# Performance work log

Measured on AMD Instinct MI355X. Metric: run time of the kernel, lower is better.

The kernel has to match this reference:

```python
import jax, jax.numpy as jnp
import numpy as np

B, N, FIN, H, F = 8, 1024, 256, 8, 64
NEG_SLOPE = 0.2


def setup_inputs() -> dict:
    key = jax.random.key(0)
    k = jax.random.split(key, 6)
    x = jax.random.normal(k[0], (B, N, FIN), dtype=jnp.float32)
    adj_mask = jax.random.randint(k[1], (B, N, N), 0, 2, dtype=jnp.int32)
    edge_prior = jax.random.normal(k[2], (B, N, N), dtype=jnp.float32)
    # params (xavier-style scales)
    W = jax.random.normal(k[3], (FIN, H * F), dtype=jnp.float32) * np.sqrt(2.0 / (FIN + H * F))
    a_left = jax.random.normal(k[4], (H, F), dtype=jnp.float32) * np.sqrt(2.0 / (1 + F))
    a_right = jax.random.normal(k[5], (H, F), dtype=jnp.float32) * np.sqrt(2.0 / (1 + F))
    edge_scale = jnp.float32(0.05)
    return {"x": x, "adj_mask": adj_mask, "edge_prior": edge_prior,
            "W": W, "a_left": a_left, "a_right": a_right, "edge_scale": edge_scale}


def reference(x, adj_mask, edge_prior, W, a_left, a_right, edge_scale):
    b, n, _ = x.shape
    h = (x @ W).reshape(b, n, H, F)                      # [B,N,H,F]
    e_left = jnp.einsum('bnhf,hf->bnh', h, a_left)       # [B,N,H]
    e_right = jnp.einsum('bnhf,hf->bnh', h, a_right)     # [B,N,H]
    e = jax.nn.leaky_relu(e_left[:, :, None, :] + e_right[:, None, :, :],
                          negative_slope=NEG_SLOPE)      # [B,N,N,H]
    e = e + edge_scale * edge_prior[..., None]
    e = jnp.where((adj_mask == 0)[..., None], -jnp.inf, e)
    alpha = jax.nn.softmax(e, axis=2)                    # softmax over neighbors j
    h_new = jnp.einsum('bijh,bjhf->bihf', alpha, h)      # [B,N,H,F]
    return h_new.reshape(b, n, H * F)                    # concat=True
```

## Files before the change

### kernel.cpp

```cpp
#include <hip/hip_runtime.h>
#include <hip/hip_bf16.h>

#define B_ 8
#define N_ 1024
#define FIN_ 256
#define H_ 8
#define F_ 64
#define HF_ 512
#define BN_ 8192
#define LOG2E 1.4426950408889634f

using bf16x8 = __attribute__((ext_vector_type(8))) short;
using f32x4  = __attribute__((ext_vector_type(4))) float;
using i32x4  = __attribute__((ext_vector_type(4))) int;

__device__ __forceinline__ short f2bf(float x) {
  __hip_bfloat16 b = __float2bfloat16(x);
  return *reinterpret_cast<short*>(&b);
}
__device__ __forceinline__ float bf2f(short s) {
  union { unsigned u; float f; } v;
  v.u = ((unsigned)(unsigned short)s) << 16;
  return v.f;
}
__device__ __forceinline__ bf16x8 cvtCE(f32x4 pa, f32x4 pb, i32x4 ma, i32x4 mb, float es) {
  bf16x8 o;
#pragma unroll
  for (int e = 0; e < 4; e++) {
    o[e]     = f2bf(ma[e] != 0 ? es * pa[e] : -1e30f);
    o[e + 4] = f2bf(mb[e] != 0 ? es * pb[e] : -1e30f);
  }
  return o;
}

__global__ __launch_bounds__(256) void k_cvt(
    const float* __restrict__ x, const float* __restrict__ W,
    short* __restrict__ xb, short* __restrict__ Wt) {
  const int bid = blockIdx.x;
  if (bid < 1024) {
    const int idx = (bid * 256 + threadIdx.x) * 8;
    f32x4 a = *(const f32x4*)(x + idx);
    f32x4 b = *(const f32x4*)(x + idx + 4);
    bf16x8 o;
    o[0]=f2bf(a[0]); o[1]=f2bf(a[1]); o[2]=f2bf(a[2]); o[3]=f2bf(a[3]);
    o[4]=f2bf(b[0]); o[5]=f2bf(b[1]); o[6]=f2bf(b[2]); o[7]=f2bf(b[3]);
    *(bf16x8*)(xb + idx) = o;
  } else {
    const int idx = (bid - 1024) * 256 + threadIdx.x;
    const int f = idx >> 8, c = idx & 255;
    Wt[f * FIN_ + c] = f2bf(W[c * HF_ + f]);
  }
}

__global__ __launch_bounds__(256) void k_h(
    const short* __restrict__ Wt, const short* __restrict__ xb,
    const float* __restrict__ aL, const float* __restrict__ aR,
    short* __restrict__ hAg, float* __restrict__ el_t, float* __restrict__ er_t) {
  const int nt = blockIdx.x;
  const int h  = blockIdx.y;
  const int w  = threadIdx.x >> 6;
  const int l  = threadIdx.x & 63;
  const int lr = l & 15, lk = l >> 4;
  const int n0 = nt * 64;
  const int fbase = h * 64 + w * 16;

  f32x4 acc[4] = {};
  const short* arow = Wt + (fbase + lr) * FIN_ + lk * 8;

#pragma unroll
  for (int k0 = 0; k0 < FIN_; k0 += 32) {
    bf16x8 a = *(const bf16x8*)(arow + k0);
#pragma unroll
    for (int nf = 0; nf < 4; nf++) {
      bf16x8 bb = *(const bf16x8*)(xb + (size_t)(n0 + nf * 16 + lr) * FIN_ + k0 + lk * 8);
      acc[nf] = __builtin_amdgcn_mfma_f32_16x16x32_bf16(a, bb, acc[nf], 0, 0, 0);
    }
  }

  __shared__ short sT[64][72];
  __shared__ float sEl[4][64], sEr[4][64];
  float al[4], ar[4];
#pragma unroll
  for (int r = 0; r < 4; r++) {
    const int fl = w * 16 + lk * 4 + r;
    al[r] = aL[h * F_ + fl];
    ar[r] = aR[h * F_ + fl];
  }
#pragma unroll
  for (int nf = 0; nf < 4; nf++) {
    const int nl = nf * 16 + lr;
#pragma unroll
    for (int r = 0; r < 4; r++)
      sT[w * 16 + lk * 4 + r][nl] = f2bf(acc[nf][r]);
    float pl = acc[nf][0]*al[0] + acc[nf][1]*al[1] + acc[nf][2]*al[2] + acc[nf][3]*al[3];
    float pr = acc[nf][0]*ar[0] + acc[nf][1]*ar[1] + acc[nf][2]*ar[2] + acc[nf][3]*ar[3];
    pl += __shfl_xor(pl, 16); pl += __shfl_xor(pl, 32);
    pr += __shfl_xor(pr, 16); pr += __shfl_xor(pr, 32);
    if (lk == 0) { sEl[w][nl] = pl; sEr[w][nl] = pr; }
  }
  __syncthreads();
  if (threadIdx.x < 64) {
    const int n = threadIdx.x;
    el_t[h * BN_ + n0 + n] = (sEl[0][n] + sEl[1][n] + sEl[2][n] + sEl[3][n]) * LOG2E;
    er_t[h * BN_ + n0 + n] = (sEr[0][n] + sEr[1][n] + sEr[2][n] + sEr[3][n]) * LOG2E;
  }
  const int b8h = (nt >> 4) * 8 + h;
  const int jb  = (nt & 15) * 2;
#pragma unroll
  for (int gi = 0; gi < 2; gi++) {
    const int g   = threadIdx.x * 2 + gi;
    const int jsl = g >> 8, ff = (g >> 6) & 3, gl = g & 63;
    const int glr = gl & 15, glk = gl >> 4;
    bf16x8 v = *(const bf16x8*)(&sT[ff * 16 + glr][jsl * 32 + glk * 8]);
    *(bf16x8*)(hAg + (((size_t)b8h * 32 + jb + jsl) * 4 + ff) * 512 + gl * 8) = v;
  }
}

#define PREF_G(sn, Hd, E0d, E1d)                                      \
  {                                                                   \
    const short* hs_ = hW + (size_t)(sn) * 2048;                      \
    Hd[0] = *(const bf16x8*)(hs_);                                    \
    Hd[1] = *(const bf16x8*)(hs_ + 512);                              \
    Hd[2] = *(const bf16x8*)(hs_ + 1024);                             \
    Hd[3] = *(const bf16x8*)(hs_ + 1536);                             \
    E0d   = *(const f32x4*)(erp + (sn) * 32);                         \
    E1d   = *(const f32x4*)(erp + (sn) * 32 + 4);                     \
  }

#define PREF_C(sn, C0d, C1d)                                          \
  {                                                                   \
    const int gi_ = (((sn) * 4 + lk) ^ xsw) * 8;                      \
    C0d = *(const bf16x8*)(cbl0 + gi_);                               \
    C1d = *(const bf16x8*)(cbl1 + gi_);                               \
  }

#define COMP2(Hu, C0u, C1u, E0u, E1u)                                          \
  {                                                                            \
    bf16x8 pfA, pfB;                                                           \
    _Pragma("unroll")                                                          \
    for (int q = 0; q < 4; q++) {                                              \
      const float e0 = E0u[q], e1 = E1u[q];                                    \
      float sA  = el0 + e0, sA2 = el0 + e1;                                    \
      float sB  = el1 + e0, sB2 = el1 + e1;                                    \
      float vA  = fmaf(0.6f, sA,  bf2f(C0u[q]));                               \
      vA  = fmaf(0.4f, fabsf(sA),  vA);                                        \
      float vA2 = fmaf(0.6f, sA2, bf2f(C0u[q + 4]));                           \
      vA2 = fmaf(0.4f, fabsf(sA2), vA2);                                       \
      float vB  = fmaf(0.6f, sB,  bf2f(C1u[q]));                               \
      vB  = fmaf(0.4f, fabsf(sB),  vB);                                        \
      float vB2 = fmaf(0.6f, sB2, bf2f(C1u[q + 4]));                           \
      vB2 = fmaf(0.4f, fabsf(sB2), vB2);                                       \
      float x1_, x2_, x3_, x4_;                                                \
      asm("v_exp_f32 %0, %1" : "=v"(x1_) : "v"(vA));                           \
      asm("v_exp_f32 %0, %1" : "=v"(x2_) : "v"(vA2));                          \
      asm("v_exp_f32 %0, %1" : "=v"(x3_) : "v"(vB));                           \
      asm("v_exp_f32 %0, %1" : "=v"(x4_) : "v"(vB2));                          \
      pfA[q] = f2bf(x1_); pfA[q + 4] = f2bf(x2_);                              \
      pfB[q] = f2bf(x3_); pfB[q + 4] = f2bf(x4_);                              \
    }                                                                          \
    accSA   = __builtin_amdgcn_mfma_f32_16x16x32_bf16(ones, pfA, accSA, 0,0,0);\
    accSB   = __builtin_amdgcn_mfma_f32_16x16x32_bf16(ones, pfB, accSB, 0,0,0);\
    accA[0] = __builtin_amdgcn_mfma_f32_16x16x32_bf16(Hu[0], pfA, accA[0],0,0,0);\
    accB[0] = __builtin_amdgcn_mfma_f32_16x16x32_bf16(Hu[0], pfB, accB[0],0,0,0);\
    accA[1] = __builtin_amdgcn_mfma_f32_16x16x32_bf16(Hu[1], pfA, accA[1],0,0,0);\
    accB[1] = __builtin_amdgcn_mfma_f32_16x16x32_bf16(Hu[1], pfB, accB[1],0,0,0);\
    accA[2] = __builtin_amdgcn_mfma_f32_16x16x32_bf16(Hu[2], pfA, accA[2],0,0,0);\
    accB[2] = __builtin_amdgcn_mfma_f32_16x16x32_bf16(Hu[2], pfB, accB[2],0,0,0);\
    accA[3] = __builtin_amdgcn_mfma_f32_16x16x32_bf16(Hu[3], pfA, accA[3],0,0,0);\
    accB[3] = __builtin_amdgcn_mfma_f32_16x16x32_bf16(Hu[3], pfB, accB[3],0,0,0);\
  }

__global__ __launch_bounds__(256, 2) void k_attn(
    const short* __restrict__ hAg, const float* __restrict__ el_t,
    const float* __restrict__ er_t, const float* __restrict__ prior,
    const int* __restrict__ mask, const float* __restrict__ esp,
    float* __restrict__ out) {
  const int bid = blockIdx.x;
  const int b  = bid & 7;
  const int hp = (bid >> 3) & 1;
  const int it = bid >> 4;
  const int t  = threadIdx.x;
  const int h  = hp * 4 + (t >> 6);
  const int l  = t & 63;
  const int lr = l & 15, lk = l >> 4;
  const int i0 = it * 32;
  const size_t bn = (size_t)b * N_;
  const float es = esp[0] * LOG2E;

  __shared__ short cbuf[33 * 1024];

  {
    const int srow = t >> 3;
    const int g0   = t & 7;
    const int sw   = srow & 7;
    const size_t grow = (bn + i0 + srow) * (size_t)N_;
    const float* pg = prior + grow;
    const int*   mg = mask  + grow;
#pragma unroll
    for (int k = 0; k < 16; k++) {
      const int g = g0 + 8 * k;
      f32x4 p0 = *(const f32x4*)(pg + g * 8), p1 = *(const f32x4*)(pg + g * 8 + 4);
      i32x4 m0 = *(const i32x4*)(mg + g * 8), m1 = *(const i32x4*)(mg + g * 8 + 4);
      *(bf16x8*)(&cbuf[srow * 1024 + (g ^ sw) * 8]) = cvtCE(p0, p1, m0, m1, es);
    }
  }

  const float el0 = el_t[h * BN_ + bn + i0 + lr];
  const float el1 = el_t[h * BN_ + bn + i0 + 16 + lr];
  const float* erp = er_t + h * BN_ + bn + lk * 8;
  const short* hW  = hAg + (size_t)(b * 8 + h) * 65536 + l * 8;
  const short* cbl0 = cbuf + lr * 1024;
  const short* cbl1 = cbuf + (16 + lr) * 1024;
  const int xsw = lr & 7;

  bf16x8 HA[4], HB[4], cA0, cA1, cB0, cB1;
  f32x4 eA0, eA1, eB0, eB1;

  PREF_G(0, HA, eA0, eA1);
  PREF_G(1, HB, eB0, eB1);

  f32x4 accA[4] = {}, accB[4] = {};
  f32x4 accSA = {}, accSB = {};
  bf16x8 ones;
#pragma unroll
  for (int e = 0; e < 8; e++) ones[e] = (short)0x3F80;

  __syncthreads();
  PREF_C(0, cA0, cA1);
  PREF_C(1, cB0, cB1);

  for (int s = 0; s < 32; s += 2) {
    COMP2(HA, cA0, cA1, eA0, eA1);
    PREF_G(s + 2, HA, eA0, eA1);
    PREF_C(s + 2, cA0, cA1);
    COMP2(HB, cB0, cB1, eB0, eB1);
    PREF_G(s + 3, HB, eB0, eB1);
    PREF_C(s + 3, cB0, cB1);
  }

  const float invA = 1.0f / accSA[0];
  const float invB = 1.0f / accSB[0];
  const size_t rowA = bn + i0 + lr;
  const size_t rowB = rowA + 16;
#pragma unroll
  for (int ff = 0; ff < 4; ff++) {
    f32x4 va = accA[ff], vb = accB[ff];
    va[0]*=invA; va[1]*=invA; va[2]*=invA; va[3]*=invA;
    vb[0]*=invB; vb[1]*=invB; vb[2]*=invB; vb[3]*=invB;
    *(f32x4*)(out + rowA * HF_ + h * 64 + ff * 16 + lk * 4) = va;
    *(f32x4*)(out + rowB * HF_ + h * 64 + ff * 16 + lk * 4) = vb;
  }
}

extern "C" void kernel_launch(void* const* d_in, const int* in_sizes, int n_in,
                              void* d_out, int out_size, void* d_ws, size_t ws_size,
                              hipStream_t stream) {
  const float* x     = (const float*)d_in[0];
  const int*   adj   = (const int*)  d_in[1];
  const float* prior = (const float*)d_in[2];
  const float* W     = (const float*)d_in[3];
  const float* aL    = (const float*)d_in[4];
  const float* aR    = (const float*)d_in[5];
  const float* es    = (const float*)d_in[6];
  float* out = (float*)d_out;

  char* ws = (char*)d_ws;
  short* hAg  = (short*)ws;
  short* xb   = (short*)(ws + 8u  * 1024 * 1024);
  short* Wt   = (short*)(ws + 12u * 1024 * 1024);
  float* el_t = (float*)(ws + 12u * 1024 * 1024 + 262144);
  float* er_t = (float*)(ws + 12u * 1024 * 1024 + 524288);

  hipLaunchKernelGGL(k_cvt, dim3(1536), dim3(256), 0, stream, x, W, xb, Wt);
  hipLaunchKernelGGL(k_h,   dim3(128, 8), dim3(256), 0, stream,
                     Wt, xb, aL, aR, hAg, el_t, er_t);
  hipLaunchKernelGGL(k_attn, dim3(512), dim3(256), 0, stream,
                     hAg, el_t, er_t, prior, adj, es, out);
}
```

Measured before the change: 65.82 us.

## Double-buffer prior/mask staging in 256-column chunks with 64-row tiles

The attention kernel now handles 64 query rows per block instead of 32, which halves the grid and doubles the reuse of each loaded H tile across four MFMA row groups. The prior/mask tile is staged in four 256-column chunks into two shared buffers, so the global loads for the next chunk are interleaved with compute on the current one. This replaces the old single up-front load of the full 32x1024 tile. MFMA blocks are wrapped in s_setprio. The risks are higher register pressure from 16 accumulators, 256 blocks possibly underfilling the CUs, and extra barriers.

New measurement: 69.87 us. 1.06x slower.

```diff
diff --git a/kernel.cpp b/kernel.cpp
--- a/kernel.cpp
+++ b/kernel.cpp
@@ -127,47 +127,71 @@
     E1d   = *(const f32x4*)(erp + (sn) * 32 + 4);                     \
   }
 
-#define PREF_C(sn, C0d, C1d)                                          \
-  {                                                                   \
-    const int gi_ = (((sn) * 4 + lk) ^ xsw) * 8;                      \
-    C0d = *(const bf16x8*)(cbl0 + gi_);                               \
-    C1d = *(const bf16x8*)(cbl1 + gi_);                               \
-  }
-
-#define COMP2(Hu, C0u, C1u, E0u, E1u)                                          \
-  {                                                                            \
-    bf16x8 pfA, pfB;                                                           \
-    _Pragma("unroll")                                                          \
-    for (int q = 0; q < 4; q++) {                                              \
-      const float e0 = E0u[q], e1 = E1u[q];                                    \
-      float sA  = el0 + e0, sA2 = el0 + e1;                                    \
-      float sB  = el1 + e0, sB2 = el1 + e1;                                    \
-      float vA  = fmaf(0.6f, sA,  bf2f(C0u[q]));                               \
-      vA  = fmaf(0.4f, fabsf(sA),  vA);                                        \
-      float vA2 = fmaf(0.6f, sA2, bf2f(C0u[q + 4]));                           \
-      vA2 = fmaf(0.4f, fabsf(sA2), vA2);                                       \
-      float vB  = fmaf(0.6f, sB,  bf2f(C1u[q]));                               \
-      vB  = fmaf(0.4f, fabsf(sB),  vB);                                        \
-      float vB2 = fmaf(0.6f, sB2, bf2f(C1u[q + 4]));                           \
-      vB2 = fmaf(0.4f, fabsf(sB2), vB2);                                       \
-      float x1_, x2_, x3_, x4_;                                                \
-      asm("v_exp_f32 %0, %1" : "=v"(x1_) : "v"(vA));                           \
-      asm("v_exp_f32 %0, %1" : "=v"(x2_) : "v"(vA2));                          \
-      asm("v_exp_f32 %0, %1" : "=v"(x3_) : "v"(vB));                           \
-      asm("v_exp_f32 %0, %1" : "=v"(x4_) : "v"(vB2));                          \
-      pfA[q] = f2bf(x1_); pfA[q + 4] = f2bf(x2_);                              \
-      pfB[q] = f2bf(x3_); pfB[q + 4] = f2bf(x4_);                              \
-    }                                                                          \
-    accSA   = __builtin_amdgcn_mfma_f32_16x16x32_bf16(ones, pfA, accSA, 0,0,0);\
-    accSB   = __builtin_amdgcn_mfma_f32_16x16x32_bf16(ones, pfB, accSB, 0,0,0);\
-    accA[0] = __builtin_amdgcn_mfma_f32_16x16x32_bf16(Hu[0], pfA, accA[0],0,0,0);\
-    accB[0] = __builtin_amdgcn_mfma_f32_16x16x32_bf16(Hu[0], pfB, accB[0],0,0,0);\
-    accA[1] = __builtin_amdgcn_mfma_f32_16x16x32_bf16(Hu[1], pfA, accA[1],0,0,0);\
-    accB[1] = __builtin_amdgcn_mfma_f32_16x16x32_bf16(Hu[1], pfB, accB[1],0,0,0);\
-    accA[2] = __builtin_amdgcn_mfma_f32_16x16x32_bf16(Hu[2], pfA, accA[2],0,0,0);\
-    accB[2] = __builtin_amdgcn_mfma_f32_16x16x32_bf16(Hu[2], pfB, accB[2],0,0,0);\
-    accA[3] = __builtin_amdgcn_mfma_f32_16x16x32_bf16(Hu[3], pfA, accA[3],0,0,0);\
-    accB[3] = __builtin_amdgcn_mfma_f32_16x16x32_bf16(Hu[3], pfB, accB[3],0,0,0);\
+#define PREF_C4(cbp, js, Cd)                                          \
+  {                                                                   \
+    const int gi_ = (((js) * 4 + lk) ^ xsw) * 8;                      \
+    Cd[0] = *(const bf16x8*)((cbp) + lr * 256 + gi_);                 \
+    Cd[1] = *(const bf16x8*)((cbp) + (16 + lr) * 256 + gi_);          \
+    Cd[2] = *(const bf16x8*)((cbp) + (32 + lr) * 256 + gi_);          \
+    Cd[3] = *(const bf16x8*)((cbp) + (48 + lr) * 256 + gi_);          \
+  }
+
+#define SLOAD(ch1, js)                                                \
+  {                                                                   \
+    const float* pp_ = rowp + (ch1) * 256 + (js) * 8;                 \
+    const int*   mm_ = rowm + (ch1) * 256 + (js) * 8;                 \
+    sp0 = *(const f32x4*)(pp_); sp1 = *(const f32x4*)(pp_ + 4);       \
+    sm0 = *(const i32x4*)(mm_); sm1 = *(const i32x4*)(mm_ + 4);       \
+  }
+
+#define SWRITE(bufp, js)                                              \
+  {                                                                   \
+    *(bf16x8*)((bufp) + rbase + (((sgrp + (js)) ^ rsw) * 8)) =        \
+        cvtCE(sp0, sp1, sm0, sm1, es);                                \
+  }
+
+#define LGT(elv, ee, cc, dst)                                         \
+  {                                                                   \
+    float t_ = (elv) + (ee);                                          \
+    float v_ = fmaf(0.4f, fabsf(t_), fmaf(0.6f, t_, bf2f(cc)));       \
+    float x_;                                                         \
+    asm("v_exp_f32 %0, %1" : "=v"(x_) : "v"(v_));                     \
+    dst = f2bf(x_);                                                   \
+  }
+
+#define COMP4(Hu, Cu, E0u, E1u)                                                 \
+  {                                                                             \
+    bf16x8 pf0, pf1, pf2, pf3;                                                  \
+    _Pragma("unroll")                                                           \
+    for (int q = 0; q < 4; q++) {                                               \
+      const float e0 = E0u[q], e1 = E1u[q];                                     \
+      LGT(el0, e0, Cu[0][q], pf0[q]); LGT(el0, e1, Cu[0][q + 4], pf0[q + 4]);   \
+      LGT(el1, e0, Cu[1][q], pf1[q]); LGT(el1, e1, Cu[1][q + 4], pf1[q + 4]);   \
+      LGT(el2, e0, Cu[2][q], pf2[q]); LGT(el2, e1, Cu[2][q + 4], pf2[q + 4]);   \
+      LGT(el3, e0, Cu[3][q], pf3[q]); LGT(el3, e1, Cu[3][q + 4], pf3[q + 4]);   \
+    }                                                                           \
+    __builtin_amdgcn_s_setprio(1);                                              \
+    accS[0] = __builtin_amdgcn_mfma_f32_16x16x32_bf16(ones, pf0, accS[0],0,0,0);\
+    accS[1] = __builtin_amdgcn_mfma_f32_16x16x32_bf16(ones, pf1, accS[1],0,0,0);\
+    accS[2] = __builtin_amdgcn_mfma_f32_16x16x32_bf16(ones, pf2, accS[2],0,0,0);\
+    accS[3] = __builtin_amdgcn_mfma_f32_16x16x32_bf16(ones, pf3, accS[3],0,0,0);\
+    acc[0][0] = __builtin_amdgcn_mfma_f32_16x16x32_bf16(Hu[0], pf0, acc[0][0],0,0,0);\
+    acc[0][1] = __builtin_amdgcn_mfma_f32_16x16x32_bf16(Hu[0], pf1, acc[0][1],0,0,0);\
+    acc[0][2] = __builtin_amdgcn_mfma_f32_16x16x32_bf16(Hu[0], pf2, acc[0][2],0,0,0);\
+    acc[0][3] = __builtin_amdgcn_mfma_f32_16x16x32_bf16(Hu[0], pf3, acc[0][3],0,0,0);\
+    acc[1][0] = __builtin_amdgcn_mfma_f32_16x16x32_bf16(Hu[1], pf0, acc[1][0],0,0,0);\
+    acc[1][1] = __builtin_amdgcn_mfma_f32_16x16x32_bf16(Hu[1], pf1, acc[1][1],0,0,0);\
+    acc[1][2] = __builtin_amdgcn_mfma_f32_16x16x32_bf16(Hu[1], pf2, acc[1][2],0,0,0);\
+    acc[1][3] = __builtin_amdgcn_mfma_f32_16x16x32_bf16(Hu[1], pf3, acc[1][3],0,0,0);\
+    acc[2][0] = __builtin_amdgcn_mfma_f32_16x16x32_bf16(Hu[2], pf0, acc[2][0],0,0,0);\
+    acc[2][1] = __builtin_amdgcn_mfma_f32_16x16x32_bf16(Hu[2], pf1, acc[2][1],0,0,0);\
+    acc[2][2] = __builtin_amdgcn_mfma_f32_16x16x32_bf16(Hu[2], pf2, acc[2][2],0,0,0);\
+    acc[2][3] = __builtin_amdgcn_mfma_f32_16x16x32_bf16(Hu[2], pf3, acc[2][3],0,0,0);\
+    acc[3][0] = __builtin_amdgcn_mfma_f32_16x16x32_bf16(Hu[3], pf0, acc[3][0],0,0,0);\
+    acc[3][1] = __builtin_amdgcn_mfma_f32_16x16x32_bf16(Hu[3], pf1, acc[3][1],0,0,0);\
+    acc[3][2] = __builtin_amdgcn_mfma_f32_16x16x32_bf16(Hu[3], pf2, acc[3][2],0,0,0);\
+    acc[3][3] = __builtin_amdgcn_mfma_f32_16x16x32_bf16(Hu[3], pf3, acc[3][3],0,0,0);\
+    __builtin_amdgcn_s_setprio(0);                                              \
   }
 
 __global__ __launch_bounds__(256, 2) void k_attn(
@@ -183,72 +207,93 @@
   const int h  = hp * 4 + (t >> 6);
   const int l  = t & 63;
   const int lr = l & 15, lk = l >> 4;
-  const int i0 = it * 32;
+  const int i0 = it * 64;
   const size_t bn = (size_t)b * N_;
   const float es = esp[0] * LOG2E;
 
-  __shared__ short cbuf[33 * 1024];
-
-  {
-    const int srow = t >> 3;
-    const int g0   = t & 7;
-    const int sw   = srow & 7;
-    const size_t grow = (bn + i0 + srow) * (size_t)N_;
-    const float* pg = prior + grow;
-    const int*   mg = mask  + grow;
-#pragma unroll
-    for (int k = 0; k < 16; k++) {
-      const int g = g0 + 8 * k;
-      f32x4 p0 = *(const f32x4*)(pg + g * 8), p1 = *(const f32x4*)(pg + g * 8 + 4);
-      i32x4 m0 = *(const i32x4*)(mg + g * 8), m1 = *(const i32x4*)(mg + g * 8 + 4);
-      *(bf16x8*)(&cbuf[srow * 1024 + (g ^ sw) * 8]) = cvtCE(p0, p1, m0, m1, es);
-    }
-  }
-
-  const float el0 = el_t[h * BN_ + bn + i0 + lr];
-  const float el1 = el_t[h * BN_ + bn + i0 + 16 + lr];
+  __shared__ short cbuf[2][16384];
+
+  const int r    = t >> 2;
+  const int sub  = t & 3;
+  const int rbase = r * 256;
+  const int rsw  = r & 7;
+  const int sgrp = sub * 8;
+  const float* rowp = prior + (bn + i0 + r) * (size_t)N_ + sub * 64;
+  const int*   rowm = mask  + (bn + i0 + r) * (size_t)N_ + sub * 64;
+  f32x4 sp0, sp1; i32x4 sm0, sm1;
+
+  const float* elh = el_t + h * BN_ + bn + i0;
+  const float el0 = elh[lr], el1 = elh[16 + lr], el2 = elh[32 + lr], el3 = elh[48 + lr];
   const float* erp = er_t + h * BN_ + bn + lk * 8;
   const short* hW  = hAg + (size_t)(b * 8 + h) * 65536 + l * 8;
-  const short* cbl0 = cbuf + lr * 1024;
-  const short* cbl1 = cbuf + (16 + lr) * 1024;
   const int xsw = lr & 7;
 
-  bf16x8 HA[4], HB[4], cA0, cA1, cB0, cB1;
+  bf16x8 HA[4], HB[4], cA[4], cB[4];
   f32x4 eA0, eA1, eB0, eB1;
-
+  f32x4 acc[4][4] = {};
+  f32x4 accS[4] = {};
+  bf16x8 ones;
+#pragma unroll
+  for (int e = 0; e < 8; e++) ones[e] = (short)0x3F80;
+
+#pragma unroll
+  for (int g = 0; g < 8; g++) {
+    SLOAD(0, g);
+    SWRITE(&cbuf[0][0], g);
+  }
   PREF_G(0, HA, eA0, eA1);
   PREF_G(1, HB, eB0, eB1);
-
-  f32x4 accA[4] = {}, accB[4] = {};
-  f32x4 accSA = {}, accSB = {};
-  bf16x8 ones;
-#pragma unroll
-  for (int e = 0; e < 8; e++) ones[e] = (short)0x3F80;
-
   __syncthreads();
-  PREF_C(0, cA0, cA1);
-  PREF_C(1, cB0, cB1);
-
-  for (int s = 0; s < 32; s += 2) {
-    COMP2(HA, cA0, cA1, eA0, eA1);
-    PREF_G(s + 2, HA, eA0, eA1);
-    PREF_C(s + 2, cA0, cA1);
-    COMP2(HB, cB0, cB1, eB0, eB1);
-    PREF_G(s + 3, HB, eB0, eB1);
-    PREF_C(s + 3, cB0, cB1);
-  }
-
-  const float invA = 1.0f / accSA[0];
-  const float invB = 1.0f / accSB[0];
-  const size_t rowA = bn + i0 + lr;
-  const size_t rowB = rowA + 16;
-#pragma unroll
-  for (int ff = 0; ff < 4; ff++) {
-    f32x4 va = accA[ff], vb = accB[ff];
-    va[0]*=invA; va[1]*=invA; va[2]*=invA; va[3]*=invA;
-    vb[0]*=invB; vb[1]*=invB; vb[2]*=invB; vb[3]*=invB;
-    *(f32x4*)(out + rowA * HF_ + h * 64 + ff * 16 + lk * 4) = va;
-    *(f32x4*)(out + rowB * HF_ + h * 64 + ff * 16 + lk * 4) = vb;
+  PREF_C4(&cbuf[0][0], 0, cA);
+  PREF_C4(&cbuf[0][0], 1, cB);
+
+  for (int ch = 0; ch < 4; ++ch) {
+    const int s0 = ch * 8;
+    const short* cbc = &cbuf[ch & 1][0];
+    short*       cbn = &cbuf[(ch + 1) & 1][0];
+    const bool stg = (ch < 3);
+    if (stg) { SLOAD(ch + 1, 0); }
+    COMP4(HA, cA, eA0, eA1);
+    PREF_G(s0 + 2, HA, eA0, eA1);  PREF_C4(cbc, 2, cA);
+    if (stg) { SWRITE(cbn, 0); SLOAD(ch + 1, 1); }
+    COMP4(HB, cB, eB0, eB1);
+    PREF_G(s0 + 3, HB, eB0, eB1);  PREF_C4(cbc, 3, cB);
+    if (stg) { SWRITE(cbn, 1); SLOAD(ch + 1, 2); }
+    COMP4(HA, cA, eA0, eA1);
+    PREF_G(s0 + 4, HA, eA0, eA1);  PREF_C4(cbc, 4, cA);
+    if (stg) { SWRITE(cbn, 2); SLOAD(ch + 1, 3); }
+    COMP4(HB, cB, eB0, eB1);
+    PREF_G(s0 + 5, HB, eB0, eB1);  PREF_C4(cbc, 5, cB);
+    if (stg) { SWRITE(cbn, 3); SLOAD(ch + 1, 4); }
+    COMP4(HA, cA, eA0, eA1);
+    PREF_G(s0 + 6, HA, eA0, eA1);  PREF_C4(cbc, 6, cA);
+    if (stg) { SWRITE(cbn, 4); SLOAD(ch + 1, 5); }
+    COMP4(HB, cB, eB0, eB1);
+    PREF_G(s0 + 7, HB, eB0, eB1);  PREF_C4(cbc, 7, cB);
+    if (stg) { SWRITE(cbn, 5); SLOAD(ch + 1, 6); }
+    COMP4(HA, cA, eA0, eA1);
+    { const int sn_ = (s0 + 8 > 31) ? 31 : s0 + 8; PREF_G(sn_, HA, eA0, eA1); }
+    if (stg) { SWRITE(cbn, 6); SLOAD(ch + 1, 7); }
+    COMP4(HB, cB, eB0, eB1);
+    { const int sn_ = (s0 + 9 > 31) ? 31 : s0 + 9; PREF_G(sn_, HB, eB0, eB1); }
+    if (stg) {
+      SWRITE(cbn, 7);
+      __syncthreads();
+      PREF_C4(cbn, 0, cA);
+      PREF_C4(cbn, 1, cB);
+    }
+  }
+
+#pragma unroll
+  for (int fi = 0; fi < 4; fi++) {
+    const float inv = 1.0f / accS[fi][0];
+    const size_t row = bn + i0 + fi * 16 + lr;
+#pragma unroll
+    for (int ff = 0; ff < 4; ff++) {
+      f32x4 v = acc[ff][fi];
+      v[0] *= inv; v[1] *= inv; v[2] *= inv; v[3] *= inv;
+      *(f32x4*)(out + row * HF_ + h * 64 + ff * 16 + lk * 4) = v;
+    }
   }
 }
 
@@ -274,6 +319,6 @@
   hipLaunchKernelGGL(k_cvt, dim3(1536), dim3(256), 0, stream, x, W, xb, Wt);
   hipLaunchKernelGGL(k_h,   dim3(128, 8), dim3(256), 0, stream,
                      Wt, xb, aL, aR, hAg, el_t, er_t);
-  hipLaunchKernelGGL(k_attn, dim3(512), dim3(256), 0, stream,
+  hipLaunchKernelGGL(k_attn, dim3(256), dim3(256), 0, stream,
                      hAg, el_t, er_t, prior, adj, es, out);
 }
```

## Precompute prior/mask bias into MFMA-layout bf16 buffer via separate kernel

Applied to the files above, without the earlier changes.

Moves the fp32 prior plus int mask to bf16 bias conversion out of the attention kernel into a new k_pre kernel. k_pre writes the bias into a global buffer already laid out in MFMA fragment order. The attention kernel then streams these fragments straight from global memory alongside h and er, with no LDS staging or __syncthreads. Its software prefetch deepens from two stages to four, and the MFMA block is wrapped in s_setprio. The intent is to remove the LDS prologue and raise occupancy. The cost is an extra kernel launch and a 16 MB bf16 write-then-read round trip through memory.

New measurement: 67.29 us. +2.2%, slower.

```diff
diff --git a/kernel.cpp b/kernel.cpp
--- a/kernel.cpp
+++ b/kernel.cpp
@@ -52,6 +52,30 @@
   }
 }
 
+__global__ __launch_bounds__(256) void k_pre(
+    const float* __restrict__ prior, const int* __restrict__ mask,
+    const float* __restrict__ esp, short* __restrict__ cmat) {
+  const int b  = blockIdx.x & 7;
+  const int it = blockIdx.x >> 3;
+  const int t  = threadIdx.x;
+  const int i  = t >> 3;
+  const int jb = (t & 7) * 8;
+  const float es = esp[0] * LOG2E;
+  const size_t rowbase = ((size_t)b * N_ + it * 32 + i) * N_;
+  short* cmt = cmat + (size_t)(b * 32 + it) * 32768
+             + (i >> 4) * 512 + (i & 15) * 8;
+#pragma unroll
+  for (int jt = 0; jt < 16; jt++) {
+    const int j = jt * 64 + jb;
+    f32x4 p0 = *(const f32x4*)(prior + rowbase + j);
+    f32x4 p1 = *(const f32x4*)(prior + rowbase + j + 4);
+    i32x4 m0 = *(const i32x4*)(mask + rowbase + j);
+    i32x4 m1 = *(const i32x4*)(mask + rowbase + j + 4);
+    *(bf16x8*)(cmt + (j >> 5) * 1024 + ((j >> 3) & 3) * 128) =
+        cvtCE(p0, p1, m0, m1, es);
+  }
+}
+
 __global__ __launch_bounds__(256) void k_h(
     const short* __restrict__ Wt, const short* __restrict__ xb,
     const float* __restrict__ aL, const float* __restrict__ aR,
@@ -116,7 +140,7 @@
   }
 }
 
-#define PREF_G(sn, Hd, E0d, E1d)                                      \
+#define PREFX(sn, Hd, E0d, E1d, Cd)                                   \
   {                                                                   \
     const short* hs_ = hW + (size_t)(sn) * 2048;                      \
     Hd[0] = *(const bf16x8*)(hs_);                                    \
@@ -125,16 +149,11 @@
     Hd[3] = *(const bf16x8*)(hs_ + 1536);                             \
     E0d   = *(const f32x4*)(erp + (sn) * 32);                         \
     E1d   = *(const f32x4*)(erp + (sn) * 32 + 4);                     \
-  }
-
-#define PREF_C(sn, C0d, C1d)                                          \
-  {                                                                   \
-    const int gi_ = (((sn) * 4 + lk) ^ xsw) * 8;                      \
-    C0d = *(const bf16x8*)(cbl0 + gi_);                               \
-    C1d = *(const bf16x8*)(cbl1 + gi_);                               \
-  }
-
-#define COMP2(Hu, C0u, C1u, E0u, E1u)                                          \
+    Cd[0] = *(const bf16x8*)(cmW + (size_t)(sn) * 1024);              \
+    Cd[1] = *(const bf16x8*)(cmW + (size_t)(sn) * 1024 + 512);        \
+  }
+
+#define COMP2(Hu, Cu, E0u, E1u)                                                \
   {                                                                            \
     bf16x8 pfA, pfB;                                                           \
     _Pragma("unroll")                                                          \
@@ -142,13 +161,13 @@
       const float e0 = E0u[q], e1 = E1u[q];                                    \
       float sA  = el0 + e0, sA2 = el0 + e1;                                    \
       float sB  = el1 + e0, sB2 = el1 + e1;                                    \
-      float vA  = fmaf(0.6f, sA,  bf2f(C0u[q]));                               \
+      float vA  = fmaf(0.6f, sA,  bf2f(Cu[0][q]));                             \
       vA  = fmaf(0.4f, fabsf(sA),  vA);                                        \
-      float vA2 = fmaf(0.6f, sA2, bf2f(C0u[q + 4]));                           \
+      float vA2 = fmaf(0.6f, sA2, bf2f(Cu[0][q + 4]));                         \
       vA2 = fmaf(0.4f, fabsf(sA2), vA2);                                       \
-      float vB  = fmaf(0.6f, sB,  bf2f(C1u[q]));                               \
+      float vB  = fmaf(0.6f, sB,  bf2f(Cu[1][q]));                             \
       vB  = fmaf(0.4f, fabsf(sB),  vB);                                        \
-      float vB2 = fmaf(0.6f, sB2, bf2f(C1u[q + 4]));                           \
+      float vB2 = fmaf(0.6f, sB2, bf2f(Cu[1][q + 4]));                         \
       vB2 = fmaf(0.4f, fabsf(sB2), vB2);                                       \
       float x1_, x2_, x3_, x4_;                                                \
       asm("v_exp_f32 %0, %1" : "=v"(x1_) : "v"(vA));                           \
@@ -158,6 +177,7 @@
       pfA[q] = f2bf(x1_); pfA[q + 4] = f2bf(x2_);                              \
       pfB[q] = f2bf(x3_); pfB[q + 4] = f2bf(x4_);                              \
     }                                                                          \
+    __builtin_amdgcn_s_setprio(1);                                             \
     accSA   = __builtin_amdgcn_mfma_f32_16x16x32_bf16(ones, pfA, accSA, 0,0,0);\
     accSB   = __builtin_amdgcn_mfma_f32_16x16x32_bf16(ones, pfB, accSB, 0,0,0);\
     accA[0] = __builtin_amdgcn_mfma_f32_16x16x32_bf16(Hu[0], pfA, accA[0],0,0,0);\
@@ -168,12 +188,12 @@
     accB[2] = __builtin_amdgcn_mfma_f32_16x16x32_bf16(Hu[2], pfB, accB[2],0,0,0);\
     accA[3] = __builtin_amdgcn_mfma_f32_16x16x32_bf16(Hu[3], pfA, accA[3],0,0,0);\
     accB[3] = __builtin_amdgcn_mfma_f32_16x16x32_bf16(Hu[3], pfB, accB[3],0,0,0);\
+    __builtin_amdgcn_s_setprio(0);                                             \
   }
 
 __global__ __launch_bounds__(256, 2) void k_attn(
     const short* __restrict__ hAg, const float* __restrict__ el_t,
-    const float* __restrict__ er_t, const float* __restrict__ prior,
-    const int* __restrict__ mask, const float* __restrict__ esp,
+    const float* __restrict__ er_t, const short* __restrict__ cmat,
     float* __restrict__ out) {
   const int bid = blockIdx.x;
   const int b  = bid & 7;
@@ -185,57 +205,32 @@
   const int lr = l & 15, lk = l >> 4;
   const int i0 = it * 32;
   const size_t bn = (size_t)b * N_;
-  const float es = esp[0] * LOG2E;
-
-  __shared__ short cbuf[33 * 1024];
-
-  {
-    const int srow = t >> 3;
-    const int g0   = t & 7;
-    const int sw   = srow & 7;
-    const size_t grow = (bn + i0 + srow) * (size_t)N_;
-    const float* pg = prior + grow;
-    const int*   mg = mask  + grow;
-#pragma unroll
-    for (int k = 0; k < 16; k++) {
-      const int g = g0 + 8 * k;
-      f32x4 p0 = *(const f32x4*)(pg + g * 8), p1 = *(const f32x4*)(pg + g * 8 + 4);
-      i32x4 m0 = *(const i32x4*)(mg + g * 8), m1 = *(const i32x4*)(mg + g * 8 + 4);
-      *(bf16x8*)(&cbuf[srow * 1024 + (g ^ sw) * 8]) = cvtCE(p0, p1, m0, m1, es);
-    }
-  }
 
   const float el0 = el_t[h * BN_ + bn + i0 + lr];
   const float el1 = el_t[h * BN_ + bn + i0 + 16 + lr];
   const float* erp = er_t + h * BN_ + bn + lk * 8;
   const short* hW  = hAg + (size_t)(b * 8 + h) * 65536 + l * 8;
-  const short* cbl0 = cbuf + lr * 1024;
-  const short* cbl1 = cbuf + (16 + lr) * 1024;
-  const int xsw = lr & 7;
-
-  bf16x8 HA[4], HB[4], cA0, cA1, cB0, cB1;
-  f32x4 eA0, eA1, eB0, eB1;
-
-  PREF_G(0, HA, eA0, eA1);
-  PREF_G(1, HB, eB0, eB1);
-
+  const short* cmW = cmat + (size_t)(b * 32 + it) * 32768 + l * 8;
+
+  bf16x8 HA[4], HB[4], HC[4], HD[4];
+  bf16x8 cA[2], cB[2], cC[2], cD[2];
+  f32x4 eA0, eA1, eB0, eB1, eC0, eC1, eD0, eD1;
   f32x4 accA[4] = {}, accB[4] = {};
   f32x4 accSA = {}, accSB = {};
   bf16x8 ones;
 #pragma unroll
   for (int e = 0; e < 8; e++) ones[e] = (short)0x3F80;
 
-  __syncthreads();
-  PREF_C(0, cA0, cA1);
-  PREF_C(1, cB0, cB1);
-
-  for (int s = 0; s < 32; s += 2) {
-    COMP2(HA, cA0, cA1, eA0, eA1);
-    PREF_G(s + 2, HA, eA0, eA1);
-    PREF_C(s + 2, cA0, cA1);
-    COMP2(HB, cB0, cB1, eB0, eB1);
-    PREF_G(s + 3, HB, eB0, eB1);
-    PREF_C(s + 3, cB0, cB1);
+  PREFX(0, HA, eA0, eA1, cA);
+  PREFX(1, HB, eB0, eB1, cB);
+  PREFX(2, HC, eC0, eC1, cC);
+  PREFX(3, HD, eD0, eD1, cD);
+
+  for (int s = 0; s < 32; s += 4) {
+    COMP2(HA, cA, eA0, eA1);  PREFX(s + 4, HA, eA0, eA1, cA);
+    COMP2(HB, cB, eB0, eB1);  PREFX(s + 5, HB, eB0, eB1, cB);
+    COMP2(HC, cC, eC0, eC1);  PREFX(s + 6, HC, eC0, eC1, cC);
+    COMP2(HD, cD, eD0, eD1);  PREFX(s + 7, HD, eD0, eD1, cD);
   }
 
   const float invA = 1.0f / accSA[0];
@@ -270,10 +265,12 @@
   short* Wt   = (short*)(ws + 12u * 1024 * 1024);
   float* el_t = (float*)(ws + 12u * 1024 * 1024 + 262144);
   float* er_t = (float*)(ws + 12u * 1024 * 1024 + 524288);
+  short* cmat = (short*)(ws + 13u * 1024 * 1024);
 
   hipLaunchKernelGGL(k_cvt, dim3(1536), dim3(256), 0, stream, x, W, xb, Wt);
+  hipLaunchKernelGGL(k_pre, dim3(256), dim3(256), 0, stream, prior, adj, es, cmat);
   hipLaunchKernelGGL(k_h,   dim3(128, 8), dim3(256), 0, stream,
                      Wt, xb, aL, aR, hAg, el_t, er_t);
   hipLaunchKernelGGL(k_attn, dim3(512), dim3(256), 0, stream,
-                     hAg, el_t, er_t, prior, adj, es, out);
-}
+                     hAg, el_t, er_t, cmat, out);
+}
```
